# Kernel tuning notes

Measured on AMD Instinct MI355X. Metric: run time of the kernel, lower is better.

The kernel has to match this reference:

```python
import jax, jax.numpy as jnp
import numpy as np

L, H, C, T, V = 6, 12, 768, 1024, 50257
HD = C // H
B = 2
EPS = 1e-5


def setup_inputs() -> dict:
    key = jax.random.key(0)
    ks = jax.random.split(key, 10)
    std = 0.02
    proj_std = 0.02 / np.sqrt(2 * L)  # specialized init for projection layers

    def n(k, shape, s=std):
        return jax.random.normal(k, shape, dtype=jnp.float32) * s

    return {
        "tokens": jax.random.randint(ks[0], (B, T), 0, V),
        "tok_emb": n(ks[1], (V, C)),
        "pos_emb": n(ks[2], (T, C)),
        # per-layer stacked params, leading dim L (scanned)
        "Wq": n(ks[3], (L, H, C, HD)),
        "Wk": n(ks[4], (L, H, C, HD)),
        "Wv": n(ks[5], (L, H, C, HD)),
        "Wo": n(ks[6], (L, C, C), proj_std),
        "bo": jnp.zeros((L, C), jnp.float32),
        "ln1_g": jnp.ones((L, C), jnp.float32),
        "ln1_b": jnp.zeros((L, C), jnp.float32),
        "ln2_g": jnp.ones((L, C), jnp.float32),
        "ln2_b": jnp.zeros((L, C), jnp.float32),
        "W1": n(ks[7], (L, C, 4 * C)),
        "b1": jnp.zeros((L, 4 * C), jnp.float32),
        "W2": n(ks[8], (L, 4 * C, C), proj_std),
        "b2": jnp.zeros((L, C), jnp.float32),
        "lnf_g": jnp.ones((C,), jnp.float32),
        "lnf_b": jnp.zeros((C,), jnp.float32),
        "head_w": n(ks[9], (C, V)),
        "head_b": jnp.zeros((V,), jnp.float32),
    }


def _ln(x, g, b):
    m = x.mean(-1, keepdims=True)
    v = ((x - m) ** 2).mean(-1, keepdims=True)
    return (x - m) * jax.lax.rsqrt(v + EPS) * g + b


def _forward(tokens, p):
    x = p["tok_emb"][tokens] + p["pos_emb"][None, : tokens.shape[1]]  # [B,T,C]
    mask = jnp.tril(jnp.ones((T, T), dtype=bool))
    scale = C ** -0.5  # NOTE: original scales by input channel C, not head_size

    def block(x, lp):
        Wq, Wk, Wv, Wo, bo, g1, b1, g2, b2, W1, bb1, W2, bb2 = lp
        # NOTE: original writes x = ln1(x); x = x + attn(x)  (residual from normed x)
        x = _ln(x, g1, b1)
        q = jnp.einsum("btc,hcd->bhtd", x, Wq)
        k = jnp.einsum("btc,hcd->bhtd", x, Wk)
        v = jnp.einsum("btc,hcd->bhtd", x, Wv)
        s = jnp.einsum("bhtd,bhsd->bhts", q, k) * scale
        s = jnp.where(mask, s, -jnp.inf)
        a = jax.nn.softmax(s, axis=-1)
        y = jnp.einsum("bhts,bhsd->bhtd", a, v)
        y = y.transpose(0, 2, 1, 3).reshape(x.shape)  # concat heads -> [B,T,C]
        x = x + y @ Wo + bo
        x = _ln(x, g2, b2)
        h = jax.nn.gelu(x @ W1 + bb1, approximate=False)  # torch GELU = exact erf
        x = x + h @ W2 + bb2
        return x, None

    lps = (p["Wq"], p["Wk"], p["Wv"], p["Wo"], p["bo"], p["ln1_g"], p["ln1_b"],
           p["ln2_g"], p["ln2_b"], p["W1"], p["b1"], p["W2"], p["b2"])
    x, _ = jax.lax.scan(block, x, lps)
    x = _ln(x, p["lnf_g"], p["lnf_b"])
    return x @ p["head_w"] + p["head_b"]  # [B,T,V]


def reference(tokens, tok_emb, pos_emb, Wq, Wk, Wv, Wo, bo, ln1_g, ln1_b,
              ln2_g, ln2_b, W1, b1, W2, b2, lnf_g, lnf_b, head_w, head_b):
    p = dict(tok_emb=tok_emb, pos_emb=pos_emb, Wq=Wq, Wk=Wk, Wv=Wv, Wo=Wo, bo=bo,
             ln1_g=ln1_g, ln1_b=ln1_b, ln2_g=ln2_g, ln2_b=ln2_b, W1=W1, b1=b1,
             W2=W2, b2=b2, lnf_g=lnf_g, lnf_b=lnf_b, head_w=head_w, head_b=head_b)
    return _forward(tokens, p)
```

## Files before the change

kernel.cpp:

```cpp
#include <hip/hip_runtime.h>
#include <hip/hip_bf16.h>
#include <stdint.h>
#include <math.h>


#define L_ 6
#define H_ 12
#define C_ 768
#define T_ 1024
#define V_ 50257
#define VP_ 50304
#define VP2_ 50432
#define HD_ 64
#define BT_ 2048
#define F_ 3072
#define SCALE_ 0.03608439182435161f
#define NEGBIG_ -1e30f

typedef __bf16 bf;
typedef __attribute__((ext_vector_type(8))) __bf16 bf16x8;
typedef __attribute__((ext_vector_type(4))) __bf16 bf16x4;
typedef __attribute__((ext_vector_type(4))) float f32x4;

__device__ __forceinline__ void gload16(const void* g, void* l) {
  __builtin_amdgcn_global_load_lds(
      (const __attribute__((address_space(1))) unsigned int*)g,
      (__attribute__((address_space(3))) unsigned int*)l, 16, 0, 0);
}

__device__ __forceinline__ float gelu_f(float x) {
  return 0.5f * x * (1.0f + erff(x * 0.70710678118654752f));
}

__global__ __launch_bounds__(256) void embed_k(const int* __restrict__ tok,
                                               const float* __restrict__ te,
                                               const float* __restrict__ pe,
                                               float* __restrict__ x) {
  int bt = blockIdx.x;
  int c = blockIdx.y * 256 + threadIdx.x;
  int t = bt & (T_ - 1);
  int v = tok[bt];
  x[(size_t)bt * C_ + c] = te[(size_t)v * C_ + c] + pe[(size_t)t * C_ + c];
}

__global__ __launch_bounds__(256) void ln_k(const float* __restrict__ xin,
                                            float* __restrict__ xout,
                                            bf* __restrict__ xb,
                                            const float* __restrict__ g,
                                            const float* __restrict__ b) {
  int row = blockIdx.x;
  const float* xr = xin + (size_t)row * C_;
  int tid = threadIdx.x;
  float v0 = xr[tid], v1 = xr[tid + 256], v2 = xr[tid + 512];
  float s1 = v0 + v1 + v2;
  float s2 = v0 * v0 + v1 * v1 + v2 * v2;
#pragma unroll
  for (int o = 32; o > 0; o >>= 1) {
    s1 += __shfl_xor(s1, o, 64);
    s2 += __shfl_xor(s2, o, 64);
  }
  __shared__ float r1[4], r2[4];
  int w = tid >> 6, lane = tid & 63;
  if (lane == 0) { r1[w] = s1; r2[w] = s2; }
  __syncthreads();
  float S1 = r1[0] + r1[1] + r1[2] + r1[3];
  float S2 = r2[0] + r2[1] + r2[2] + r2[3];
  float mean = S1 * (1.0f / C_);
  float var = S2 * (1.0f / C_) - mean * mean;
  float rs = rsqrtf(fmaxf(var, 0.0f) + 1e-5f);
  float* xo = xout + (size_t)row * C_;
  bf* xbo = xb + (size_t)row * C_;
  float vv[3] = {v0, v1, v2};
#pragma unroll
  for (int j = 0; j < 3; ++j) {
    int c = tid + j * 256;
    float o = (vv[j] - mean) * rs * g[c] + b[c];
    xo[c] = o;
    xbo[c] = (bf)o;
  }
}

__device__ __forceinline__ void transpose_body(const float* __restrict__ src,
                                               bf* __restrict__ dst, int src_ld,
                                               int dst_ld, int k0, int n0,
                                               int nmax) {
  __shared__ __align__(16) bf tl[64][72];
  int tid = threadIdx.x;
  int r = tid >> 2;
  int cb = (tid & 3) * 16;
#pragma unroll
  for (int j4 = 0; j4 < 4; ++j4) {
    int c = cb + j4 * 4;
    int n = n0 + c;
    size_t idx = (size_t)(k0 + r) * src_ld + n;
    const float* sp = src + idx;
    if (n + 4 <= nmax && (idx & 3) == 0) {
      f32x4 v = *(const f32x4*)sp;
      tl[r][c] = (bf)v[0];
      tl[r][c + 1] = (bf)v[1];
      tl[r][c + 2] = (bf)v[2];
      tl[r][c + 3] = (bf)v[3];
    } else {
#pragma unroll
      for (int j = 0; j < 4; ++j)
        tl[r][c + j] = (n + j < nmax) ? (bf)sp[j] : (bf)0.0f;
    }
  }
  __syncthreads();
  int n = n0 + r;
  bf16x8 w0, w1;
#pragma unroll
  for (int j = 0; j < 8; ++j) {
    w0[j] = tl[cb + j][r];
    w1[j] = tl[cb + 8 + j][r];
  }
  bf* dp = dst + (size_t)n * dst_ld + k0 + cb;
  *(bf16x8*)dp = w0;
  *(bf16x8*)(dp + 8) = w1;
}

__global__ __launch_bounds__(256) void transpose_k(const float* __restrict__ src,
                                                   bf* __restrict__ dst,
                                                   int src_ld, int dst_ld,
                                                   int nmax) {
  transpose_body(src, dst, src_ld, dst_ld, blockIdx.x * 64, blockIdx.y * 64,
                 nmax);
}

__global__ __launch_bounds__(256) void trans_layer_k(
    const float* __restrict__ Wq, const float* __restrict__ Wk,
    const float* __restrict__ Wv, const float* __restrict__ Wo,
    const float* __restrict__ W1, const float* __restrict__ W2,
    bf* __restrict__ wqkvT, bf* __restrict__ woT, bf* __restrict__ w1T,
    bf* __restrict__ w2T) {
  int r = blockIdx.x;
  if (r < 432) {
    int z = r / 12, k0 = (r % 12) * 64;
    int tsel = z / H_, hh = z % H_;
    const float* W = (tsel == 0) ? Wq : (tsel == 1) ? Wk : Wv;
    transpose_body(W + (size_t)hh * C_ * HD_,
                   wqkvT + (size_t)(tsel * C_ + hh * HD_) * C_, HD_, C_, k0, 0,
                   HD_);
  } else if (r < 576) {
    r -= 432;
    transpose_body(Wo, woT, C_, C_, (r % 12) * 64, (r / 12) * 64, C_);
  } else if (r < 1152) {
    r -= 576;
    transpose_body(W1, w1T, F_, C_, (r % 12) * 64, (r / 12) * 64, F_);
  } else {
    r -= 1152;
    transpose_body(W2, w2T, C_, F_, (r % 48) * 64, (r / 48) * 64, C_);
  }
}

template <int MODE, int BM, int BN, int NW>
__global__ __launch_bounds__(NW * 64) void gemm_bt(
    const bf* __restrict__ A, const bf* __restrict__ Bt,
    const float* __restrict__ bias, float* __restrict__ xres,
    bf* __restrict__ o0, bf* __restrict__ o1, bf* __restrict__ o2, int K) {
  constexpr int WM = BM / 2;
  constexpr int WN = BN / (NW / 2);
  constexpr int MI = WM / 16, NJ = WN / 16;
  constexpr int HALF = (BM + BN) * 64;
  __shared__ __align__(16) bf smem[2 * HALF];
  const int tid = threadIdx.x;
  const int w = tid >> 6, lane = tid & 63;
  const int wm = (NW == 8) ? (w >> 2) : (w >> 1);
  const int wn = (NW == 8) ? (w & 3) : (w & 1);
  const int lm = lane & 15, lg = lane >> 4;

  const int lin = blockIdx.y * gridDim.x + blockIdx.x;
  const int q8 = (gridDim.x * gridDim.y) >> 3;
  const int wg = (lin & 7) * q8 + (lin >> 3);
  const int mt = gridDim.y;
  const int m0 = (wg % mt) * BM, n0 = (wg / mt) * BN;

  const int lr8 = lane >> 3;
  const int lc8s = ((lane & 7) ^ lr8) * 8;

  auto stage = [&](int buf, int k0) {
    bf* aL = smem + buf * HALF;
    bf* bL = aL + BM * 64;
#pragma unroll
    for (int c = 0; c < BM / (8 * NW); ++c) {
      int row = c * (8 * NW) + w * 8;
      gload16(A + (size_t)(m0 + row + lr8) * K + k0 + lc8s, &aL[row * 64]);
    }
#pragma unroll
    for (int c = 0; c < BN / (8 * NW); ++c) {
      int row = c * (8 * NW) + w * 8;
      gload16(Bt + (size_t)(n0 + row + lr8) * K + k0 + lc8s, &bL[row * 64]);
    }
  };

  f32x4 acc[MI][NJ];
#pragma unroll
  for (int i = 0; i < MI; ++i)
#pragma unroll
    for (int j = 0; j < NJ; ++j) acc[i][j] = (f32x4){0.f, 0.f, 0.f, 0.f};

  const int cXor = (lm & 7) * 8;
  const int NT = K >> 6;
  stage(0, 0);
  __syncthreads();
  int cur = 0;
  for (int t = 0; t < NT; ++t) {
    if (t + 1 < NT) stage(cur ^ 1, (t + 1) << 6);
    const bf* aL = smem + cur * HALF;
    const bf* bL = aL + BM * 64;
#pragma unroll
    for (int ks = 0; ks < 2; ++ks) {
      const int cc = (ks * 32 + lg * 8) ^ cXor;
      bf16x8 af[MI], bfv[NJ];
#pragma unroll
      for (int i = 0; i < MI; ++i)
        af[i] = *(const bf16x8*)&aL[(wm * WM + i * 16 + lm) * 64 + cc];
#pragma unroll
      for (int j = 0; j < NJ; ++j)
        bfv[j] = *(const bf16x8*)&bL[(wn * WN + j * 16 + lm) * 64 + cc];
      __builtin_amdgcn_s_setprio(1);
#pragma unroll
      for (int i = 0; i < MI; ++i)
#pragma unroll
        for (int j = 0; j < NJ; ++j)
          acc[i][j] = __builtin_amdgcn_mfma_f32_16x16x32_bf16(
              af[i], bfv[j], acc[i][j], 0, 0, 0);
      __builtin_amdgcn_s_setprio(0);
    }
    __syncthreads();
    cur ^= 1;
  }

  if constexpr (MODE == 3) {
    int ngj[NJ];
    float bv[NJ];
#pragma unroll
    for (int j = 0; j < NJ; ++j) {
      ngj[j] = n0 + wn * WN + j * 16 + lm;
      bv[j] = (ngj[j] < V_) ? bias[ngj[j]] : 0.f;
    }
#pragma unroll
    for (int i = 0; i < MI; ++i)
#pragma unroll
      for (int r = 0; r < 4; ++r) {
        int row = m0 + wm * WM + i * 16 + lg * 4 + r;
        float* orow = xres + (size_t)row * V_;
#pragma unroll
        for (int j = 0; j < NJ; ++j)
          if (ngj[j] < V_) orow[ngj[j]] = acc[i][j][r] + bv[j];
      }
    return;
  }

  if constexpr (MODE == 0) {
    const int bb = m0 >> 10;
    if (n0 >= 2 * C_) {
      bf* sv = smem;
#pragma unroll
      for (int i = 0; i < MI; ++i)
#pragma unroll
        for (int j = 0; j < NJ; ++j) {
          int dl = wn * WN + j * 16 + lm;
#pragma unroll
          for (int r = 0; r < 4; ++r) {
            int tl = wm * WM + i * 16 + lg * 4 + r;
            sv[dl * (BM + 8) + tl] = (bf)acc[i][j][r];
          }
        }
      __syncthreads();
      int dd_l = tid >> 1, half = tid & 1;
      size_t vrow = (size_t)bb * C_ + (n0 - 2 * C_) + dd_l;
      int t_base = m0 & (T_ - 1);
#pragma unroll
      for (int s = 0; s < 4; ++s) {
        int tt = half * 32 + s * 8;
        *(bf16x8*)(o2 + vrow * T_ + t_base + tt) =
            *(const bf16x8*)&sv[dd_l * (BM + 8) + tt];
      }
      return;
    }
    bf* dst = (n0 < C_) ? o0 : o1;
    int nb = (n0 < C_) ? n0 : n0 - C_;
    size_t basej[NJ];
#pragma unroll
    for (int j = 0; j < NJ; ++j) {
      int rr = nb + wn * WN + j * 16 + lm;
      int hh = rr >> 6, dd = rr & 63;
      basej[j] = ((size_t)(bb * H_ + hh) * T_) * HD_ + dd;
    }
#pragma unroll
    for (int i = 0; i < MI; ++i)
#pragma unroll
      for (int r = 0; r < 4; ++r) {
        int tt = (m0 + wm * WM + i * 16 + lg * 4 + r) & (T_ - 1);
#pragma unroll
        for (int j = 0; j < NJ; ++j)
          dst[basej[j] + (size_t)tt * HD_] = (bf)acc[i][j][r];
      }
    return;
  }

  int ngj[NJ];
  float bv[NJ];
#pragma unroll
  for (int j = 0; j < NJ; ++j) {
    ngj[j] = n0 + wn * WN + j * 16 + lm;
    bv[j] = bias[ngj[j]];
  }
#pragma unroll
  for (int i = 0; i < MI; ++i)
#pragma unroll
    for (int r = 0; r < 4; ++r) {
      int row = m0 + wm * WM + i * 16 + lg * 4 + r;
      if constexpr (MODE == 1) {
        float* xrow = xres + (size_t)row * C_;
#pragma unroll
        for (int j = 0; j < NJ; ++j) xrow[ngj[j]] += acc[i][j][r] + bv[j];
      } else {
        bf* orow = o0 + (size_t)row * F_;
#pragma unroll
        for (int j = 0; j < NJ; ++j)
          orow[ngj[j]] = (bf)gelu_f(acc[i][j][r] + bv[j]);
      }
    }
}

__global__ __launch_bounds__(128) void attn_k(const bf* __restrict__ q,
                                              const bf* __restrict__ k,
                                              const bf* __restrict__ vt,
                                              bf* __restrict__ yb) {
  const int qb = blockIdx.x, bh = blockIdx.y;
  const int tid = threadIdx.x, w = tid >> 6, lane = tid & 63;
  const int lm = lane & 15, lg = lane >> 4;
  const int bb = bh / H_, hh = bh % H_;
  __shared__ __align__(16) bf kl[2][64 * 64];
  __shared__ __align__(16) bf vl[2][64 * 64];
  __shared__ __align__(16) bf pl[2][16 * 64];

  auto stage = [&](int buf, int kb) {
#pragma unroll
    for (int c = 0; c < 4; ++c) {
      int rbase = w * 32 + c * 8;
      gload16(k + ((size_t)bh * T_ + kb * 64 + rbase + lane / 8) * HD_ +
                  (lane % 8) * 8,
              &kl[buf][rbase * 64]);
      gload16(vt + ((size_t)bh * HD_ + rbase + lane / 8) * T_ + kb * 64 +
                  (lane % 8) * 8,
              &vl[buf][rbase * 64]);
    }
  };

  const int qrow = qb * 32 + w * 16 + lm;
  const bf* qbase = q + ((size_t)bh * T_ + qrow) * HD_;
  bf16x8 qf0 = *(const bf16x8*)(qbase + lg * 8);
  bf16x8 qf1 = *(const bf16x8*)(qbase + 32 + lg * 8);

  f32x4 y[4];
#pragma unroll
  for (int i = 0; i < 4; ++i) y[i] = (f32x4){0.f, 0.f, 0.f, 0.f};
  float m_run = NEGBIG_, l_run = 0.f;

  const int kbmax = qb >> 1;
  stage(0, 0);
  __syncthreads();
  int cur = 0;
  for (int kb = 0; kb <= kbmax; ++kb) {
    if (kb < kbmax) stage(cur ^ 1, kb + 1);

    f32x4 s[4];
    __builtin_amdgcn_s_setprio(1);
#pragma unroll
    for (int t = 0; t < 4; ++t) {
      s[t] = (f32x4){0.f, 0.f, 0.f, 0.f};
      bf16x8 a0 = *(const bf16x8*)&kl[cur][(t * 16 + lm) * 64 + lg * 8];
      s[t] = __builtin_amdgcn_mfma_f32_16x16x32_bf16(a0, qf0, s[t], 0, 0, 0);
      bf16x8 a1 = *(const bf16x8*)&kl[cur][(t * 16 + lm) * 64 + 32 + lg * 8];
      s[t] = __builtin_amdgcn_mfma_f32_16x16x32_bf16(a1, qf1, s[t], 0, 0, 0);
    }
    __builtin_amdgcn_s_setprio(0);

    float mx = NEGBIG_;
#pragma unroll
    for (int t = 0; t < 4; ++t)
#pragma unroll
      for (int r = 0; r < 4; ++r) {
        float v = s[t][r] * SCALE_;
        int kv = kb * 64 + t * 16 + lg * 4 + r;
        if (kv > qrow) v = NEGBIG_;
        s[t][r] = v;
        mx = fmaxf(mx, v);
      }
    mx = fmaxf(mx, __shfl_xor(mx, 16, 64));
    mx = fmaxf(mx, __shfl_xor(mx, 32, 64));
    float mnew = fmaxf(m_run, mx);
    float corr = __expf(m_run - mnew);
    float rs = 0.f;
#pragma unroll
    for (int t = 0; t < 4; ++t)
#pragma unroll
      for (int r = 0; r < 4; ++r) {
        float p = __expf(s[t][r] - mnew);
        s[t][r] = p;
        rs += p;
      }
    rs += __shfl_xor(rs, 16, 64);
    rs += __shfl_xor(rs, 32, 64);
    l_run = l_run * corr + rs;
    m_run = mnew;

#pragma unroll
    for (int t = 0; t < 4; ++t) {
      bf16x4 pk;
#pragma unroll
      for (int r = 0; r < 4; ++r) pk[r] = (bf)s[t][r];
      *(bf16x4*)&pl[w][lm * 64 + t * 16 + lg * 4] = pk;
    }

    float cy0 = __shfl(corr, lg * 4 + 0, 64);
    float cy1 = __shfl(corr, lg * 4 + 1, 64);
    float cy2 = __shfl(corr, lg * 4 + 2, 64);
    float cy3 = __shfl(corr, lg * 4 + 3, 64);
#pragma unroll
    for (int nt = 0; nt < 4; ++nt) {
      y[nt][0] *= cy0;
      y[nt][1] *= cy1;
      y[nt][2] *= cy2;
      y[nt][3] *= cy3;
    }

    __builtin_amdgcn_s_setprio(1);
#pragma unroll
    for (int nt = 0; nt < 4; ++nt)
#pragma unroll
      for (int ks = 0; ks < 2; ++ks) {
        bf16x8 ap = *(const bf16x8*)&pl[w][lm * 64 + ks * 32 + lg * 8];
        bf16x8 bv =
            *(const bf16x8*)&vl[cur][(nt * 16 + lm) * 64 + ks * 32 + lg * 8];
        y[nt] = __builtin_amdgcn_mfma_f32_16x16x32_bf16(ap, bv, y[nt], 0, 0, 0);
      }
    __builtin_amdgcn_s_setprio(0);
    __syncthreads();
    cur ^= 1;
  }

  float ly[4];
#pragma unroll
  for (int r = 0; r < 4; ++r) ly[r] = __shfl(l_run, lg * 4 + r, 64);
#pragma unroll
  for (int nt = 0; nt < 4; ++nt) {
    int cc = hh * 64 + nt * 16 + lm;
#pragma unroll
    for (int r = 0; r < 4; ++r) {
      int qr = qb * 32 + w * 16 + lg * 4 + r;
      yb[((size_t)(bb * T_ + qr)) * C_ + cc] = (bf)(y[nt][r] / ly[r]);
    }
  }
}

extern "C" void kernel_launch(void* const* d_in, const int* in_sizes, int n_in,
                              void* d_out, int out_size, void* d_ws,
                              size_t ws_size, hipStream_t stream) {
  (void)in_sizes; (void)n_in; (void)out_size; (void)ws_size;
  const int* tokens = (const int*)d_in[0];
  const float* tok_emb = (const float*)d_in[1];
  const float* pos_emb = (const float*)d_in[2];
  const float* Wq = (const float*)d_in[3];
  const float* Wk = (const float*)d_in[4];
  const float* Wv = (const float*)d_in[5];
  const float* Wo = (const float*)d_in[6];
  const float* bo = (const float*)d_in[7];
  const float* ln1g = (const float*)d_in[8];
  const float* ln1b = (const float*)d_in[9];
  const float* ln2g = (const float*)d_in[10];
  const float* ln2b = (const float*)d_in[11];
  const float* W1 = (const float*)d_in[12];
  const float* b1 = (const float*)d_in[13];
  const float* W2 = (const float*)d_in[14];
  const float* b2 = (const float*)d_in[15];
  const float* lnfg = (const float*)d_in[16];
  const float* lnfb = (const float*)d_in[17];
  const float* headw = (const float*)d_in[18];
  const float* headb = (const float*)d_in[19];
  float* out = (float*)d_out;

  uint8_t* base = (uint8_t*)d_ws;
  size_t off = 0;
  auto alloc = [&](size_t n) -> uint8_t* {
    uint8_t* r = base + off;
    off += (n + 255) & ~(size_t)255;
    return r;
  };
  float* x = (float*)alloc((size_t)BT_ * C_ * 4);
  bf* xb = (bf*)alloc((size_t)BT_ * C_ * 2);
  bf* qq = (bf*)alloc((size_t)BT_ * C_ * 2);
  bf* kk = (bf*)alloc((size_t)BT_ * C_ * 2);
  bf* vt = (bf*)alloc((size_t)BT_ * C_ * 2);
  bf* ybuf = (bf*)alloc((size_t)BT_ * C_ * 2);
  bf* hb = (bf*)alloc((size_t)BT_ * F_ * 2);
  bf* wqkvT = (bf*)alloc((size_t)3 * C_ * C_ * 2);
  bf* woT = (bf*)alloc((size_t)C_ * C_ * 2);
  bf* w1T = (bf*)alloc((size_t)F_ * C_ * 2);
  bf* w2T = (bf*)alloc((size_t)C_ * F_ * 2);
  bf* headT = (bf*)alloc((size_t)VP2_ * C_ * 2);

  dim3 blk(256), blk8(512), blk2(128);
  transpose_k<<<dim3(C_ / 64, VP2_ / 64), blk, 0, stream>>>(headw, headT, V_,
                                                            C_, V_);
  embed_k<<<dim3(BT_, 3), blk, 0, stream>>>(tokens, tok_emb, pos_emb, x);

  for (int l = 0; l < L_; ++l) {
    trans_layer_k<<<1728, blk, 0, stream>>>(
        Wq + (size_t)l * H_ * C_ * HD_, Wk + (size_t)l * H_ * C_ * HD_,
        Wv + (size_t)l * H_ * C_ * HD_, Wo + (size_t)l * C_ * C_,
        W1 + (size_t)l * C_ * F_, W2 + (size_t)l * F_ * C_, wqkvT, woT, w1T,
        w2T);

    ln_k<<<BT_, blk, 0, stream>>>(x, x, xb, ln1g + l * C_, ln1b + l * C_);
    gemm_bt<0, 64, 128, 4><<<dim3(2304 / 128, BT_ / 64), blk, 0, stream>>>(
        xb, wqkvT, nullptr, nullptr, qq, kk, vt, C_);
    attn_k<<<dim3(T_ / 32, 2 * H_), blk2, 0, stream>>>(qq, kk, vt, ybuf);
    gemm_bt<1, 64, 64, 4><<<dim3(C_ / 64, BT_ / 64), blk, 0, stream>>>(
        ybuf, woT, bo + l * C_, x, nullptr, nullptr, nullptr, C_);
    ln_k<<<BT_, blk, 0, stream>>>(x, x, xb, ln2g + l * C_, ln2b + l * C_);
    gemm_bt<2, 128, 128, 8><<<dim3(F_ / 128, BT_ / 128), blk8, 0, stream>>>(
        xb, w1T, b1 + l * F_, nullptr, hb, nullptr, nullptr, C_);
    gemm_bt<1, 64, 64, 4><<<dim3(C_ / 64, BT_ / 64), blk, 0, stream>>>(
        hb, w2T, b2 + l * C_, x, nullptr, nullptr, nullptr, F_);
  }

  ln_k<<<BT_, blk, 0, stream>>>(x, x, xb, lnfg, lnfb);
  gemm_bt<3, 256, 256, 8><<<dim3(VP2_ / 256, BT_ / 256), blk8, 0, stream>>>(
      xb, headT, headb, out, nullptr, nullptr, nullptr, C_);
}
```

Measured before the change: 1.255 ms.

## Triple-buffer LM head GEMM with explicit vmcnt waits and smaller M tile

```diff
diff --git a/kernel.cpp b/kernel.cpp
--- a/kernel.cpp
+++ b/kernel.cpp
@@ -9,7 +9,6 @@
 #define C_ 768
 #define T_ 1024
 #define V_ 50257
-#define VP_ 50304
 #define VP2_ 50432
 #define HD_ 64
 #define BT_ 2048
@@ -153,7 +152,7 @@
   }
 }
 
-template <int MODE, int BM, int BN, int NW>
+template <int MODE, int BM, int BN, int NW, int DEPTH>
 __global__ __launch_bounds__(NW * 64) void gemm_bt(
     const bf* __restrict__ A, const bf* __restrict__ Bt,
     const float* __restrict__ bias, float* __restrict__ xres,
@@ -162,7 +161,8 @@
   constexpr int WN = BN / (NW / 2);
   constexpr int MI = WM / 16, NJ = WN / 16;
   constexpr int HALF = (BM + BN) * 64;
-  __shared__ __align__(16) bf smem[2 * HALF];
+  constexpr int NBUF = (DEPTH == 2) ? 3 : 2;
+  __shared__ __align__(16) bf smem[NBUF * HALF];
   const int tid = threadIdx.x;
   const int w = tid >> 6, lane = tid & 63;
   const int wm = (NW == 8) ? (w >> 2) : (w >> 1);
@@ -201,13 +201,8 @@
 
   const int cXor = (lm & 7) * 8;
   const int NT = K >> 6;
-  stage(0, 0);
-  __syncthreads();
-  int cur = 0;
-  for (int t = 0; t < NT; ++t) {
-    if (t + 1 < NT) stage(cur ^ 1, (t + 1) << 6);
-    const bf* aL = smem + cur * HALF;
-    const bf* bL = aL + BM * 64;
+
+  auto compute = [&](const bf* aL, const bf* bL) {
 #pragma unroll
     for (int ks = 0; ks < 2; ++ks) {
       const int cc = (ks * 32 + lg * 8) ^ cXor;
@@ -227,8 +222,40 @@
               af[i], bfv[j], acc[i][j], 0, 0, 0);
       __builtin_amdgcn_s_setprio(0);
     }
+  };
+
+  if constexpr (DEPTH == 2) {
+    static_assert((BM + BN) / (8 * NW) == 6, "vmcnt constants assume LPW=6");
+    stage(0, 0);
+    if (NT > 1) stage(1, 64);
+    for (int t = 0; t < NT; ++t) {
+      if (t + 2 < NT) {
+        stage((t + 2) % 3, (t + 2) << 6);
+        asm volatile("s_waitcnt vmcnt(12)" ::: "memory");
+      } else if (t + 1 < NT) {
+        asm volatile("s_waitcnt vmcnt(6)" ::: "memory");
+      } else {
+        asm volatile("s_waitcnt vmcnt(0)" ::: "memory");
+      }
+      __builtin_amdgcn_s_barrier();
+      asm volatile("" ::: "memory");
+      const bf* aL = smem + (t % 3) * HALF;
+      compute(aL, aL + BM * 64);
+      asm volatile("" ::: "memory");
+      __builtin_amdgcn_s_barrier();
+      asm volatile("" ::: "memory");
+    }
+  } else {
+    stage(0, 0);
     __syncthreads();
-    cur ^= 1;
+    int cur = 0;
+    for (int t = 0; t < NT; ++t) {
+      if (t + 1 < NT) stage(cur ^ 1, (t + 1) << 6);
+      const bf* aL = smem + cur * HALF;
+      compute(aL, aL + BM * 64);
+      __syncthreads();
+      cur ^= 1;
+    }
   }
 
   if constexpr (MODE == 3) {
@@ -516,19 +543,19 @@
         w2T);
 
     ln_k<<<BT_, blk, 0, stream>>>(x, x, xb, ln1g + l * C_, ln1b + l * C_);
-    gemm_bt<0, 64, 128, 4><<<dim3(2304 / 128, BT_ / 64), blk, 0, stream>>>(
+    gemm_bt<0, 64, 128, 4, 1><<<dim3(2304 / 128, BT_ / 64), blk, 0, stream>>>(
         xb, wqkvT, nullptr, nullptr, qq, kk, vt, C_);
     attn_k<<<dim3(T_ / 32, 2 * H_), blk2, 0, stream>>>(qq, kk, vt, ybuf);
-    gemm_bt<1, 64, 64, 4><<<dim3(C_ / 64, BT_ / 64), blk, 0, stream>>>(
+    gemm_bt<1, 64, 64, 4, 1><<<dim3(C_ / 64, BT_ / 64), blk, 0, stream>>>(
         ybuf, woT, bo + l * C_, x, nullptr, nullptr, nullptr, C_);
     ln_k<<<BT_, blk, 0, stream>>>(x, x, xb, ln2g + l * C_, ln2b + l * C_);
-    gemm_bt<2, 128, 128, 8><<<dim3(F_ / 128, BT_ / 128), blk8, 0, stream>>>(
+    gemm_bt<2, 128, 128, 8, 1><<<dim3(F_ / 128, BT_ / 128), blk8, 0, stream>>>(
         xb, w1T, b1 + l * F_, nullptr, hb, nullptr, nullptr, C_);
-    gemm_bt<1, 64, 64, 4><<<dim3(C_ / 64, BT_ / 64), blk, 0, stream>>>(
+    gemm_bt<1, 64, 64, 4, 1><<<dim3(C_ / 64, BT_ / 64), blk, 0, stream>>>(
         hb, w2T, b2 + l * C_, x, nullptr, nullptr, nullptr, F_);
   }
 
   ln_k<<<BT_, blk, 0, stream>>>(x, x, xb, lnfg, lnfb);
-  gemm_bt<3, 256, 256, 8><<<dim3(VP2_ / 256, BT_ / 256), blk8, 0, stream>>>(
+  gemm_bt<3, 128, 256, 8, 2><<<dim3(VP2_ / 256, BT_ / 128), blk8, 0, stream>>>(
       xb, headT, headb, out, nullptr, nullptr, nullptr, C_);
 }
```

After: 1.303 ms. +3.8%, slower.
